# Performance work log

Hardware: AMD Instinct MI355X
Metric: run time of the kernel (lower is better)

The kernel has to match this reference:

```python
import jax, jax.numpy as jnp
import numpy as np

B, CIN, COUT, H, W, K = 32, 256, 256, 64, 64, 3


def setup_inputs() -> dict:
    key = jax.random.key(0)
    k1, k2, k3 = jax.random.split(key, 3)
    x = jax.random.normal(k1, (B, CIN, H, W), dtype=jnp.float32)
    # kaiming_uniform_ with a=sqrt(5): bound = sqrt(6 / ((1 + a^2) * fan_in)) = sqrt(1/fan_in)
    fan_in = CIN * K * K
    bound = float(np.sqrt(1.0 / fan_in))
    weight = jax.random.uniform(k2, (COUT, CIN, K, K), dtype=jnp.float32,
                                minval=-bound, maxval=bound)
    bias = jax.random.normal(k3, (COUT,), dtype=jnp.float32)
    return {"x": x, "weight": weight, "bias": bias}


def reference(x, weight, bias):
    # CustomConvnd with kernel=3, stride=1, padding=1 (module doubles it, pad
    # helper splits around center -> 1 element each side, zero padding),
    # equivalent to a standard 2D cross-correlation like torch Conv2d.
    out = jax.lax.conv_general_dilated(
        x, weight,
        window_strides=(1, 1),
        padding=((1, 1), (1, 1)),
        dimension_numbers=("NCHW", "OIHW", "NCHW"),
    )
    return out + bias[None, :, None, None]
```

## Files before the change

### kernel.cpp

```cpp
#include <hip/hip_runtime.h>
#include <hip/hip_bf16.h>

typedef __attribute__((ext_vector_type(8))) short short8;
typedef __attribute__((ext_vector_type(16))) float floatx16;

#define BDIM 512

constexpr int kCIN = 256, kCOUT = 256, kH = 64, kW = 64;
constexpr int BK = 32;
constexpr int NCHUNK = kCIN / BK;
constexpr int ROWS = 4;
constexpr int XR = ROWS + 2, XC = 66, NPIX = XR * XC;
constexpr int HW = kH * kW;
constexpr int NSTEP = NCHUNK * 9;

__device__ __forceinline__ int swz16(int row, int g) {
    return ((g ^ ((row >> 1) & 3)) << 4);
}

__device__ __forceinline__ unsigned short f2bf(float f) {
    unsigned u = __float_as_uint(f);
    u += 0x7fffu + ((u >> 16) & 1u);
    return (unsigned short)(u >> 16);
}

__global__ void wt_transform_kernel(const float* __restrict__ wsrc,
                                    unsigned short* __restrict__ wt) {
    int idx = blockIdx.x * 256 + threadIdx.x;
    if (idx >= 9 * 256 * 256) return;
    int ci = idx & 255;
    int co = (idx >> 8) & 255;
    int kk = idx >> 16;
    wt[idx] = f2bf(wsrc[(co * 256 + ci) * 9 + kk]);
}

__global__ __launch_bounds__(BDIM, 2)
void conv3x3_mfma_kernel(const float* __restrict__ x,
                         const unsigned short* __restrict__ wt,
                         const float* __restrict__ bias,
                         float* __restrict__ out) {
    __shared__ __align__(16) char xs[NPIX * 64];
    __shared__ __align__(16) char ws[2][256 * 64];

    const int bid = blockIdx.x;
    const int b  = bid >> 4;
    const int h0 = (bid & 15) * ROWS;

    const int tid = threadIdx.x;
    const int wv  = tid >> 6;
    const int l   = tid & 63;
    const int l31 = l & 31;
    const int hi2 = l >> 5;
    const int cog  = (wv & 1) * 128;
    const int wrow = wv >> 1;

    const float* xb = x + (size_t)b * kCIN * HW;

    floatx16 acc[4][2] = {};

    auto stageW = [&](int st) {
        int chunk = st / 9, kk = st - chunk * 9;
        const unsigned short* wp = wt + (size_t)kk * 65536 + chunk * BK;
        char* wbuf = ws[st & 1];
        #pragma unroll
        for (int it = 0; it < 2; ++it) {
            int row0 = it * 128 + wv * 16;
            int co = row0 + (l >> 2);
            int g  = (l & 3) ^ ((co >> 1) & 3);
            const unsigned short* src = wp + co * 256 + g * 8;
            __builtin_amdgcn_global_load_lds(
                (const __attribute__((address_space(1))) unsigned int*)src,
                (__attribute__((address_space(3))) unsigned int*)(wbuf + row0 * 64),
                16, 0, 0);
        }
    };

    auto stageX = [&](int chunk) {
        const int ci0 = chunk * BK;
        for (int t = tid; t < NPIX * 4; t += BDIM) {
            int g = t / NPIX;
            int rem = t - g * NPIX;
            int r = rem / XC;
            int c = rem - r * XC;
            int ih = h0 - 1 + r;
            int iw = c - 1;
            float v[8];
            if ((unsigned)ih < (unsigned)kH && (unsigned)iw < (unsigned)kW) {
                const float* p = xb + (size_t)(ci0 + g * 8) * HW + ih * kW + iw;
                #pragma unroll
                for (int j = 0; j < 8; ++j) v[j] = p[(size_t)j * HW];
            } else {
                #pragma unroll
                for (int j = 0; j < 8; ++j) v[j] = 0.f;
            }
            union { short8 s8; unsigned short u[8]; } pk;
            #pragma unroll
            for (int j = 0; j < 8; ++j) pk.u[j] = f2bf(v[j]);
            int pix = r * XC + c;
            *(short8*)(xs + pix * 64 + swz16(pix, g)) = pk.s8;
        }
    };

    stageX(0);
    stageW(0);
    __syncthreads();

    for (int st = 0; st < NSTEP; ++st) {
        const int chunk = st / 9;
        const int kk = st - chunk * 9;
        if (st < NSTEP - 1) stageW(st + 1);

        const char* wbuf = ws[st & 1];
        const int kh = kk / 3, kwo = kk - kh * 3;
        const int r = wrow + kh;

        short8 a[2][4], bfr[2][2];
        #pragma unroll
        for (int s = 0; s < 2; ++s) {
            const int g = s * 2 + hi2;
            #pragma unroll
            for (int i = 0; i < 4; ++i) {
                int co = cog + i * 32 + l31;
                a[s][i] = *(const short8*)(wbuf + co * 64 + swz16(co, g));
            }
            #pragma unroll
            for (int f = 0; f < 2; ++f) {
                int pix = r * XC + f * 32 + l31 + kwo;
                bfr[s][f] = *(const short8*)(xs + pix * 64 + swz16(pix, g));
            }
        }
        #pragma unroll
        for (int s = 0; s < 2; ++s)
            #pragma unroll
            for (int i = 0; i < 4; ++i)
                #pragma unroll
                for (int f = 0; f < 2; ++f)
                    acc[i][f] = __builtin_amdgcn_mfma_f32_32x32x16_bf16(
                        a[s][i], bfr[s][f], acc[i][f], 0, 0, 0);
        __syncthreads();

        if (kk == 8 && st < NSTEP - 1) {
            stageX(chunk + 1);
            __syncthreads();
        }
    }

    float* op = out + (size_t)b * kCOUT * HW + (size_t)(h0 + wrow) * kW;
    #pragma unroll
    for (int i = 0; i < 4; ++i) {
        #pragma unroll
        for (int rg = 0; rg < 16; ++rg) {
            int co = cog + i * 32 + (rg & 3) + 8 * (rg >> 2) + 4 * hi2;
            float bv = bias[co];
            #pragma unroll
            for (int f = 0; f < 2; ++f) {
                op[(size_t)co * HW + f * 32 + l31] = acc[i][f][rg] + bv;
            }
        }
    }
}

extern "C" void kernel_launch(void* const* d_in, const int* in_sizes, int n_in,
                              void* d_out, int out_size, void* d_ws, size_t ws_size,
                              hipStream_t stream) {
    const float* x    = (const float*)d_in[0];
    const float* wsrc = (const float*)d_in[1];
    const float* bias = (const float*)d_in[2];
    float* out = (float*)d_out;
    unsigned short* wt = (unsigned short*)d_ws;

    hipLaunchKernelGGL(wt_transform_kernel, dim3((9 * 256 * 256 + 255) / 256),
                       dim3(256), 0, stream, wsrc, wt);

    hipLaunchKernelGGL(conv3x3_mfma_kernel, dim3(32 * (kH / ROWS)), dim3(BDIM),
                       0, stream, x, wt, bias, out);
}
```

Baseline: 198.0 us.

## Split LDS tiles into per-k-group planes and pre-block weights for contiguous staging

Replaces the XOR-swizzled 64-byte-row LDS layout for both the input tile and the weight tile with four separate 16-byte-per-row planes, one per group of 8 input channels. The weight transform kernel now writes weights in a [kk][chunk][g][co][8] blocked order, so each global_load_lds fetch is fully contiguous and needs no swizzle arithmetic. The step loop also tracks chunk and kk incrementally instead of dividing by 9. The aim is to cut address arithmetic and keep LDS reads bank-conflict-free through plane separation, at the risk of new bank conflicts now that the swizzle is gone.

```diff
diff --git a/kernel.cpp b/kernel.cpp
--- a/kernel.cpp
+++ b/kernel.cpp
@@ -14,9 +14,9 @@
 constexpr int HW = kH * kW;
 constexpr int NSTEP = NCHUNK * 9;
 
-__device__ __forceinline__ int swz16(int row, int g) {
-    return ((g ^ ((row >> 1) & 3)) << 4);
-}
+constexpr int XS_PLANE = NPIX * 16;
+constexpr int WS_PLANE = 256 * 16;
+constexpr int WS_BUF   = 4 * WS_PLANE;
 
 __device__ __forceinline__ unsigned short f2bf(float f) {
     unsigned u = __float_as_uint(f);
@@ -25,22 +25,25 @@
 }
 
 __global__ void wt_transform_kernel(const float* __restrict__ wsrc,
-                                    unsigned short* __restrict__ wt) {
+                                    unsigned short* __restrict__ wt2) {
     int idx = blockIdx.x * 256 + threadIdx.x;
     if (idx >= 9 * 256 * 256) return;
-    int ci = idx & 255;
-    int co = (idx >> 8) & 255;
+    int j  = idx & 7;
+    int co = (idx >> 3) & 255;
+    int g  = (idx >> 11) & 3;
+    int chunk = (idx >> 13) & 7;
     int kk = idx >> 16;
-    wt[idx] = f2bf(wsrc[(co * 256 + ci) * 9 + kk]);
+    int ci = chunk * 32 + g * 8 + j;
+    wt2[idx] = f2bf(wsrc[(co * 256 + ci) * 9 + kk]);
 }
 
 __global__ __launch_bounds__(BDIM, 2)
 void conv3x3_mfma_kernel(const float* __restrict__ x,
-                         const unsigned short* __restrict__ wt,
+                         const unsigned short* __restrict__ wt2,
                          const float* __restrict__ bias,
                          float* __restrict__ out) {
-    __shared__ __align__(16) char xs[NPIX * 64];
-    __shared__ __align__(16) char ws[2][256 * 64];
+    __shared__ __align__(16) char xs[4 * XS_PLANE];
+    __shared__ __align__(16) char ws[2 * WS_BUF];
 
     const int bid = blockIdx.x;
     const int b  = bid >> 4;
@@ -58,19 +61,19 @@
 
     floatx16 acc[4][2] = {};
 
-    auto stageW = [&](int st) {
-        int chunk = st / 9, kk = st - chunk * 9;
-        const unsigned short* wp = wt + (size_t)kk * 65536 + chunk * BK;
-        char* wbuf = ws[st & 1];
+    auto stageW = [&](int st, int chunk, int kk) {
+        char* wbuf = ws + (st & 1) * WS_BUF;
+        const unsigned short* wp = wt2 + (size_t)(kk * 8 + chunk) * 8192;
         #pragma unroll
         for (int it = 0; it < 2; ++it) {
-            int row0 = it * 128 + wv * 16;
-            int co = row0 + (l >> 2);
-            int g  = (l & 3) ^ ((co >> 1) & 3);
-            const unsigned short* src = wp + co * 256 + g * 8;
+            int c = wv * 2 + it;
+            int g = c >> 2;
+            int row0 = (c & 3) * 64;
+            const unsigned short* src = wp + (g * 256 + row0 + l) * 8;
             __builtin_amdgcn_global_load_lds(
                 (const __attribute__((address_space(1))) unsigned int*)src,
-                (__attribute__((address_space(3))) unsigned int*)(wbuf + row0 * 64),
+                (__attribute__((address_space(3))) unsigned int*)
+                    (wbuf + g * WS_PLANE + row0 * 16),
                 16, 0, 0);
         }
     };
@@ -97,20 +100,21 @@
             #pragma unroll
             for (int j = 0; j < 8; ++j) pk.u[j] = f2bf(v[j]);
             int pix = r * XC + c;
-            *(short8*)(xs + pix * 64 + swz16(pix, g)) = pk.s8;
+            *(short8*)(xs + g * XS_PLANE + pix * 16) = pk.s8;
         }
     };
 
     stageX(0);
-    stageW(0);
+    stageW(0, 0, 0);
     __syncthreads();
 
+    int chunk = 0, kk = 0;
     for (int st = 0; st < NSTEP; ++st) {
-        const int chunk = st / 9;
-        const int kk = st - chunk * 9;
-        if (st < NSTEP - 1) stageW(st + 1);
+        int kk1 = kk + 1, chunk1 = chunk;
+        if (kk1 == 9) { kk1 = 0; chunk1++; }
+        if (st < NSTEP - 1) stageW(st + 1, chunk1, kk1);
 
-        const char* wbuf = ws[st & 1];
+        const char* wbuf = ws + (st & 1) * WS_BUF;
         const int kh = kk / 3, kwo = kk - kh * 3;
         const int r = wrow + kh;
 
@@ -121,12 +125,12 @@
             #pragma unroll
             for (int i = 0; i < 4; ++i) {
                 int co = cog + i * 32 + l31;
-                a[s][i] = *(const short8*)(wbuf + co * 64 + swz16(co, g));
+                a[s][i] = *(const short8*)(wbuf + g * WS_PLANE + co * 16);
             }
             #pragma unroll
             for (int f = 0; f < 2; ++f) {
                 int pix = r * XC + f * 32 + l31 + kwo;
-                bfr[s][f] = *(const short8*)(xs + pix * 64 + swz16(pix, g));
+                bfr[s][f] = *(const short8*)(xs + g * XS_PLANE + pix * 16);
             }
         }
         #pragma unroll
@@ -140,9 +144,10 @@
         __syncthreads();
 
         if (kk == 8 && st < NSTEP - 1) {
-            stageX(chunk + 1);
+            stageX(chunk1);
             __syncthreads();
         }
+        kk = kk1; chunk = chunk1;
     }
 
     float* op = out + (size_t)b * kCOUT * HW + (size_t)(h0 + wrow) * kW;
@@ -167,11 +172,11 @@
     const float* wsrc = (const float*)d_in[1];
     const float* bias = (const float*)d_in[2];
     float* out = (float*)d_out;
-    unsigned short* wt = (unsigned short*)d_ws;
+    unsigned short* wt2 = (unsigned short*)d_ws;
 
     hipLaunchKernelGGL(wt_transform_kernel, dim3((9 * 256 * 256 + 255) / 256),
-                       dim3(256), 0, stream, wsrc, wt);
+                       dim3(256), 0, stream, wsrc, wt2);
 
     hipLaunchKernelGGL(conv3x3_mfma_kernel, dim3(32 * (kH / ROWS)), dim3(BDIM),
-                       0, stream, x, wt, bias, out);
+                       0, stream, x, wt2, bias, out);
 }
```

Measured after the change: 192.5 us. 1.03x faster.
